# Performance work log

Measured on AMD Instinct MI355X. Metric: run time of the kernel, lower is better.

## Reference

```python
import jax, jax.numpy as jnp
import numpy as np

H = 51  # n_hidden
B = 8192  # batch
T = 2048  # seq_len
FUTURE = 64


def setup_inputs() -> dict:
    key = jax.random.key(0)
    ks = jax.random.split(key, 12)
    s = 1.0 / np.sqrt(H)
    u = lambda k, shape: jax.random.uniform(k, shape, jnp.float32, -s, s)
    return {
        "x": jax.random.normal(ks[0], (B, T), jnp.float32),
        "W_ih1": u(ks[1], (4 * H, 1)),
        "W_hh1": u(ks[2], (4 * H, H)),
        "b_ih1": u(ks[3], (4 * H,)),
        "b_hh1": u(ks[4], (4 * H,)),
        "W_ih2": u(ks[5], (4 * H, H)),
        "W_hh2": u(ks[6], (4 * H, H)),
        "b_ih2": u(ks[7], (4 * H,)),
        "b_hh2": u(ks[8], (4 * H,)),
        "W_out": u(ks[9], (1, H)),
        "b_out": u(ks[10], (1,)),
        "future": FUTURE,
    }


def _lstm_cell(x, h, c, Wih, Whh, bih, bhh):
    # PyTorch LSTMCell: gates ordered i, f, g, o
    g = x @ Wih.T + h @ Whh.T + (bih + bhh)  # [B, 4H]
    i, f, gg, o = jnp.split(g, 4, axis=-1)
    i = jax.nn.sigmoid(i)
    f = jax.nn.sigmoid(f)
    gg = jnp.tanh(gg)
    o = jax.nn.sigmoid(o)
    c2 = f * c + i * gg
    h2 = o * jnp.tanh(c2)
    return h2, c2


def reference(x, W_ih1, W_hh1, b_ih1, b_hh1, W_ih2, W_hh2, b_ih2, b_hh2,
              W_out, b_out, future):
    Bn = x.shape[0]
    h1 = jnp.zeros((Bn, H), x.dtype)
    c1 = jnp.zeros((Bn, H), x.dtype)

    def emit(h1, c1):
        # Quirk of the original code: layer-2 state is layer-1's CURRENT (h1, c1),
        # and layer-2's own state is never carried forward.
        h2, _ = _lstm_cell(h1, h1, c1, W_ih2, W_hh2, b_ih2, b_hh2)
        return h2 @ W_out.T + b_out  # [B, 1]

    def step(carry, xt):
        h1, c1 = carry
        h1, c1 = _lstm_cell(xt, h1, c1, W_ih1, W_hh1, b_ih1, b_hh1)
        out = emit(h1, c1)
        return (h1, c1), out

    xs = jnp.swapaxes(x, 0, 1)[:, :, None]  # [T, B, 1]
    (h1, c1), outs = jax.lax.scan(step, (h1, c1), xs)
    outs = outs[..., 0].T  # [B, T]

    def fstep(carry, _):
        h1, c1, out = carry
        h1, c1 = _lstm_cell(out, h1, c1, W_ih1, W_hh1, b_ih1, b_hh1)
        out = emit(h1, c1)
        return (h1, c1, out), out

    last = outs[:, -1:]
    _, fouts = jax.lax.scan(fstep, (h1, c1, last), None, length=future)
    fouts = fouts[..., 0].T if future > 0 else jnp.zeros((Bn, 0), x.dtype)
    return jnp.concatenate([outs, fouts], axis=1)  # [B, T + future]
```

## Files before the change

### kernel.cpp

```cpp
#include <hip/hip_runtime.h>

#define HH   51
#define H4   204
#define TSEQ 2048
#define FUT  64
#define TT   (TSEQ + FUT)
#define RPB  16
#define NTH  1024
#define HSTR 80

typedef _Float16 h8 __attribute__((ext_vector_type(8)));
typedef float    f4 __attribute__((ext_vector_type(4)));

#define LOG2E 1.44269504f

__device__ __forceinline__ float sigm_f(float z) {
    return __builtin_amdgcn_rcpf(1.0f + __builtin_amdgcn_exp2f(-LOG2E * z));
}
__device__ __forceinline__ float tanh_f(float z) {
    return __builtin_fmaf(2.0f,
        __builtin_amdgcn_rcpf(1.0f + __builtin_amdgcn_exp2f(-2.0f * LOG2E * z)), -1.0f);
}

__global__ __launch_bounds__(NTH, 8)
void lstm_kernel(const float* __restrict__ x,
                 const float* __restrict__ Wih1, const float* __restrict__ Whh1,
                 const float* __restrict__ bih1, const float* __restrict__ bhh1,
                 const float* __restrict__ Wih2, const float* __restrict__ Whh2,
                 const float* __restrict__ bih2, const float* __restrict__ bhh2,
                 const float* __restrict__ Wout, const float* __restrict__ bout,
                 float* __restrict__ out)
{
    __shared__ _Float16 hbuf[2][RPB][HSTR];
    __shared__ float part[2][13][17];
    __shared__ float wouts[64];

    const int tid  = threadIdx.x;
    const int lane = tid & 63;
    const int w    = tid >> 6;
    const int quad = lane >> 4;
    const int nl   = lane & 15;
    const int rb   = blockIdx.x * RPB;

    if (tid < 64) wouts[tid] = (tid < HH) ? Wout[tid] : 0.0f;
    for (int i = tid; i < 2 * RPB * HSTR; i += NTH) (&hbuf[0][0][0])[i] = (_Float16)0.0f;
    __syncthreads();
    if (tid < RPB) {
        hbuf[0][tid][0]  = (_Float16)x[(size_t)(rb + tid) * TSEQ];
        hbuf[0][tid][52] = (_Float16)1.0f;  hbuf[0][tid][53] = (_Float16)1.0f;
        hbuf[1][tid][52] = (_Float16)1.0f;  hbuf[1][tid][53] = (_Float16)1.0f;
    }
    const float bo = bout[0];

    h8 W1[2], W2[2];
    if (w < 13) {
        const int jp = 16 * w + nl;
        const int kk = jp >> 2, q = jp & 3;
        const bool valid = (jp < H4);
        const int jrow = q * HH + kk;
        float b1 = 0.0f, b2 = 0.0f;
        if (valid) { b1 = bih1[jrow] + bhh1[jrow]; b2 = bih2[jrow] + bhh2[jrow]; }
        const _Float16 b1h = (_Float16)b1, b2h = (_Float16)b2;
        const _Float16 b1l = (_Float16)(b1 - (float)b1h), b2l = (_Float16)(b2 - (float)b2h);
        #pragma unroll
        for (int s = 0; s < 2; ++s) {
            h8 w1v, w2v;
            #pragma unroll
            for (int j = 0; j < 8; ++j) {
                const int k = s * 32 + quad * 8 + j;
                _Float16 a1 = (_Float16)0.0f, a2 = (_Float16)0.0f;
                if (valid) {
                    if (k == 0) {
                        a1 = (_Float16)Wih1[jrow];
                    } else if (k <= HH) {
                        const int o = jrow * HH + (k - 1);
                        a1 = (_Float16)Whh1[o];
                        a2 = (_Float16)(Wih2[o] + Whh2[o]);
                    } else if (k == 52) { a1 = b1h; a2 = b2h; }
                    else if (k == 53)   { a1 = b1l; a2 = b2l; }
                }
                w1v[j] = a1;
                w2v[j] = a2;
            }
            W1[s] = w1v;
            W2[s] = w2v;
        }
    }

    float xnext = 0.0f;
    if (w == 14 && lane < RPB) xnext = x[(size_t)(rb + lane) * TSEQ + 1];

    const int kh = 4 * w + quad;
    float c1 = 0.0f;
    __syncthreads();

    for (int t = 0; t < TT; ++t) {
        const int cur = t & 1, nxt = cur ^ 1;

        if (w < 13) {
            const h8 Bh0 = *(const h8*)&hbuf[cur][nl][quad * 8];
            const h8 Bh1 = *(const h8*)&hbuf[cur][nl][32 + quad * 8];
            f4 g = {0.f, 0.f, 0.f, 0.f};
            g = __builtin_amdgcn_mfma_f32_16x16x32_f16(W1[0], Bh0, g, 0, 0, 0);
            g = __builtin_amdgcn_mfma_f32_16x16x32_f16(W1[1], Bh1, g, 0, 0, 0);
            const float ig = sigm_f(g[0]);
            const float fg = sigm_f(g[1]);
            const float gg = tanh_f(g[2]);
            const float og = sigm_f(g[3]);
            c1 = fg * c1 + ig * gg;
            const float h1v = og * tanh_f(c1);
            if (kh < HH) hbuf[nxt][nl][1 + kh] = (_Float16)h1v;
        } else if (w == 13) {
            if (t >= 1 && t <= TSEQ - 1 && lane < RPB) {
                float s = bo;
                #pragma unroll
                for (int j = 0; j < 13; ++j) s += part[cur ^ 1][j][lane];
                out[(size_t)(rb + lane) * TT + (t - 1)] = s;
            }
        } else if (w == 14) {
            if (lane < RPB) {
                if (t + 1 < TSEQ) hbuf[nxt][lane][0] = (_Float16)xnext;
                if (t + 2 < TSEQ) xnext = x[(size_t)(rb + lane) * TSEQ + (t + 2)];
            }
        }
        __syncthreads();

        if (w < 13) {
            const h8 Bh0 = *(const h8*)&hbuf[nxt][nl][quad * 8];
            const h8 Bh1 = *(const h8*)&hbuf[nxt][nl][32 + quad * 8];
            f4 g = {0.f, 0.f, 0.f, 0.f};
            g = __builtin_amdgcn_mfma_f32_16x16x32_f16(W2[0], Bh0, g, 0, 0, 0);
            g = __builtin_amdgcn_mfma_f32_16x16x32_f16(W2[1], Bh1, g, 0, 0, 0);
            const float ig = sigm_f(g[0]);
            const float fg = sigm_f(g[1]);
            const float gg = tanh_f(g[2]);
            const float og = sigm_f(g[3]);
            const float c2 = fg * c1 + ig * gg;
            float p = og * tanh_f(c2) * wouts[kh];
            p += __shfl_xor(p, 16, 64);
            p += __shfl_xor(p, 32, 64);
            if (quad == 0) part[cur][w][nl] = p;
        }
        __syncthreads();

        if (t >= TSEQ - 1) {
            if (w == 13 && lane < RPB) {
                float s = bo;
                #pragma unroll
                for (int j = 0; j < 13; ++j) s += part[cur][j][lane];
                out[(size_t)(rb + lane) * TT + t] = s;
                hbuf[nxt][lane][0] = (_Float16)s;
            }
            __syncthreads();
        }
    }
}

extern "C" void kernel_launch(void* const* d_in, const int* in_sizes, int n_in,
                              void* d_out, int out_size, void* d_ws, size_t ws_size,
                              hipStream_t stream) {
    (void)in_sizes; (void)n_in; (void)d_ws; (void)ws_size; (void)out_size;
    const float* x    = (const float*)d_in[0];
    const float* Wih1 = (const float*)d_in[1];
    const float* Whh1 = (const float*)d_in[2];
    const float* bih1 = (const float*)d_in[3];
    const float* bhh1 = (const float*)d_in[4];
    const float* Wih2 = (const float*)d_in[5];
    const float* Whh2 = (const float*)d_in[6];
    const float* bih2 = (const float*)d_in[7];
    const float* bhh2 = (const float*)d_in[8];
    const float* Wout = (const float*)d_in[9];
    const float* bout = (const float*)d_in[10];
    float* outp = (float*)d_out;

    dim3 grid(8192 / RPB);
    dim3 block(NTH);
    hipLaunchKernelGGL(lstm_kernel, grid, block, 0, stream,
                       x, Wih1, Whh1, bih1, bhh1, Wih2, Whh2, bih2, bhh2,
                       Wout, bout, outp);
}
```

Before: 2.961 ms.

## Merge layer-1 and layer-2 LSTM phases into one barrier per step

```diff
diff --git a/kernel.cpp b/kernel.cpp
--- a/kernel.cpp
+++ b/kernel.cpp
@@ -13,14 +13,57 @@
 typedef float    f4 __attribute__((ext_vector_type(4)));
 
 #define LOG2E 1.44269504f
-
-__device__ __forceinline__ float sigm_f(float z) {
-    return __builtin_amdgcn_rcpf(1.0f + __builtin_amdgcn_exp2f(-LOG2E * z));
+#define MFMA(a, b, c) __builtin_amdgcn_mfma_f32_16x16x32_f16(a, b, c, 0, 0, 0)
+
+__device__ __forceinline__ void act_cell(const f4 g, float cin, float* cout, float* hout) {
+    const float ei = __builtin_amdgcn_exp2f(-LOG2E * g[0]);
+    const float ef = __builtin_amdgcn_exp2f(-LOG2E * g[1]);
+    const float eg = __builtin_amdgcn_exp2f(-2.0f * LOG2E * g[2]);
+    const float eo = __builtin_amdgcn_exp2f(-LOG2E * g[3]);
+    const float A = 1.0f + ei, B = 1.0f + ef, G = 1.0f + eg, C = 1.0f + eo;
+    const float rAB = __builtin_amdgcn_rcpf(A * B);
+    const float ig = rAB * B;
+    const float fg = rAB * A;
+    const float rGC = __builtin_amdgcn_rcpf(G * C);
+    const float og = rGC * G;
+    const float tg = __builtin_fmaf(2.0f, rGC * C, -1.0f);
+    const float c2 = __builtin_fmaf(fg, cin, ig * tg);
+    const float ec = __builtin_amdgcn_exp2f(-2.0f * LOG2E * c2);
+    const float th = __builtin_fmaf(2.0f, __builtin_amdgcn_rcpf(1.0f + ec), -1.0f);
+    *cout = c2;
+    *hout = og * th;
 }
-__device__ __forceinline__ float tanh_f(float z) {
-    return __builtin_fmaf(2.0f,
-        __builtin_amdgcn_rcpf(1.0f + __builtin_amdgcn_exp2f(-2.0f * LOG2E * z)), -1.0f);
-}
+
+#define MERGED_BODY(P, EMIT_IDX, DO_EMIT, XI)                                      \
+    do {                                                                           \
+        if (is_comp) {                                                             \
+            const h8 b0 = *(const h8*)&hbuf[P][nl][quad * 8];                      \
+            const h8 b1 = *(const h8*)&hbuf[P][nl][32 + quad * 8];                 \
+            f4 G1 = {0.f, 0.f, 0.f, 0.f}, G2 = {0.f, 0.f, 0.f, 0.f};               \
+            G2 = MFMA(W2[0], b0, G2); G2 = MFMA(W2[1], b1, G2);                    \
+            G1 = MFMA(W1[0], b0, G1); G1 = MFMA(W1[1], b1, G1);                    \
+            float c2v, h2v;                                                        \
+            act_cell(G2, c1, &c2v, &h2v);         \
+            float p = h2v * wo;                                                    \
+            p += __shfl_xor(p, 16, 64);                                            \
+            p += __shfl_xor(p, 32, 64);                                            \
+            if (quad == 0) part[(P) ^ 1][cw][nl] = p;                              \
+            float hv;                                                              \
+            act_cell(G1, c1, &c1, &hv);                     \
+            if (kh < HH) hbuf[(P) ^ 1][nl][1 + kh] = (_Float16)hv;                 \
+        } else if (w == we) {                                                      \
+            if ((DO_EMIT) && lane < RPB) {                                         \
+                float s = bo;                                                      \
+                _Pragma("unroll")                                                  \
+                for (int j = 0; j < 13; ++j) s += part[P][j][lane];                \
+                out[(size_t)(rb + lane) * TT + (EMIT_IDX)] = s;                    \
+            }                                                                      \
+        } else if (w == wp && lane < RPB) {                                        \
+            if ((XI) + 1 < TSEQ) hbuf[(P) ^ 1][lane][0] = (_Float16)xnext;         \
+            if ((XI) + 2 < TSEQ) xnext = x[(size_t)(rb + lane) * TSEQ + (XI) + 2]; \
+        }                                                                          \
+        __syncthreads();                                                           \
+    } while (0)
 
 __global__ __launch_bounds__(NTH, 8)
 void lstm_kernel(const float* __restrict__ x,
@@ -42,6 +85,12 @@
     const int nl   = lane & 15;
     const int rb   = blockIdx.x * RPB;
 
+    const int  rot     = (blockIdx.x >> 8) & 1;
+    const int  cw      = w - (rot ? 3 : 0);
+    const bool is_comp = (cw >= 0) && (cw < 13);
+    const int  we      = rot ? 0 : 13;
+    const int  wp      = rot ? 1 : 14;
+
     if (tid < 64) wouts[tid] = (tid < HH) ? Wout[tid] : 0.0f;
     for (int i = tid; i < 2 * RPB * HSTR; i += NTH) (&hbuf[0][0][0])[i] = (_Float16)0.0f;
     __syncthreads();
@@ -53,8 +102,8 @@
     const float bo = bout[0];
 
     h8 W1[2], W2[2];
-    if (w < 13) {
-        const int jp = 16 * w + nl;
+    if (is_comp) {
+        const int jp = 16 * cw + nl;
         const int kk = jp >> 2, q = jp & 3;
         const bool valid = (jp < H4);
         const int jrow = q * HH + kk;
@@ -88,68 +137,71 @@
     }
 
     float xnext = 0.0f;
-    if (w == 14 && lane < RPB) xnext = x[(size_t)(rb + lane) * TSEQ + 1];
-
-    const int kh = 4 * w + quad;
+    if (w == wp && lane < RPB) xnext = x[(size_t)(rb + lane) * TSEQ + 1];
+
+    const int kh = 4 * cw + quad;
     float c1 = 0.0f;
     __syncthreads();
-
-    for (int t = 0; t < TT; ++t) {
-        const int cur = t & 1, nxt = cur ^ 1;
-
-        if (w < 13) {
-            const h8 Bh0 = *(const h8*)&hbuf[cur][nl][quad * 8];
-            const h8 Bh1 = *(const h8*)&hbuf[cur][nl][32 + quad * 8];
-            f4 g = {0.f, 0.f, 0.f, 0.f};
-            g = __builtin_amdgcn_mfma_f32_16x16x32_f16(W1[0], Bh0, g, 0, 0, 0);
-            g = __builtin_amdgcn_mfma_f32_16x16x32_f16(W1[1], Bh1, g, 0, 0, 0);
-            const float ig = sigm_f(g[0]);
-            const float fg = sigm_f(g[1]);
-            const float gg = tanh_f(g[2]);
-            const float og = sigm_f(g[3]);
-            c1 = fg * c1 + ig * gg;
-            const float h1v = og * tanh_f(c1);
-            if (kh < HH) hbuf[nxt][nl][1 + kh] = (_Float16)h1v;
-        } else if (w == 13) {
-            if (t >= 1 && t <= TSEQ - 1 && lane < RPB) {
-                float s = bo;
-                #pragma unroll
-                for (int j = 0; j < 13; ++j) s += part[cur ^ 1][j][lane];
-                out[(size_t)(rb + lane) * TT + (t - 1)] = s;
-            }
-        } else if (w == 14) {
-            if (lane < RPB) {
-                if (t + 1 < TSEQ) hbuf[nxt][lane][0] = (_Float16)xnext;
-                if (t + 2 < TSEQ) xnext = x[(size_t)(rb + lane) * TSEQ + (t + 2)];
-            }
-        }
-        __syncthreads();
-
-        if (w < 13) {
-            const h8 Bh0 = *(const h8*)&hbuf[nxt][nl][quad * 8];
-            const h8 Bh1 = *(const h8*)&hbuf[nxt][nl][32 + quad * 8];
-            f4 g = {0.f, 0.f, 0.f, 0.f};
-            g = __builtin_amdgcn_mfma_f32_16x16x32_f16(W2[0], Bh0, g, 0, 0, 0);
-            g = __builtin_amdgcn_mfma_f32_16x16x32_f16(W2[1], Bh1, g, 0, 0, 0);
-            const float ig = sigm_f(g[0]);
-            const float fg = sigm_f(g[1]);
-            const float gg = tanh_f(g[2]);
-            const float og = sigm_f(g[3]);
-            const float c2 = fg * c1 + ig * gg;
-            float p = og * tanh_f(c2) * wouts[kh];
+    const float wo = is_comp ? wouts[kh] : 0.0f;
+
+    if (is_comp) {
+        const h8 b0 = *(const h8*)&hbuf[0][nl][quad * 8];
+        const h8 b1 = *(const h8*)&hbuf[0][nl][32 + quad * 8];
+        f4 G1 = {0.f, 0.f, 0.f, 0.f};
+        G1 = MFMA(W1[0], b0, G1); G1 = MFMA(W1[1], b1, G1);
+        float hv;
+        act_cell(G1, c1, &c1, &hv);
+        if (kh < HH) hbuf[1][nl][1 + kh] = (_Float16)hv;
+    } else if (w == wp && lane < RPB) {
+        hbuf[1][lane][0] = (_Float16)xnext;
+        xnext = x[(size_t)(rb + lane) * TSEQ + 2];
+    }
+    __syncthreads();
+
+    MERGED_BODY(1, 0, false, 1);
+
+    for (int i = 2; i < TSEQ; i += 2) {
+        MERGED_BODY(0, i - 2, true, i);
+        MERGED_BODY(1, i - 1, true, i + 1);
+    }
+
+    for (int t = TSEQ - 1; t < TT; ++t) {
+        const int pb = (t + 1) & 1;
+        if (is_comp) {
+            const h8 b0 = *(const h8*)&hbuf[pb][nl][quad * 8];
+            const h8 b1 = *(const h8*)&hbuf[pb][nl][32 + quad * 8];
+            f4 G2 = {0.f, 0.f, 0.f, 0.f};
+            G2 = MFMA(W2[0], b0, G2); G2 = MFMA(W2[1], b1, G2);
+            float c2v, h2v;
+            act_cell(G2, c1, &c2v, &h2v);
+            float p = h2v * wo;
             p += __shfl_xor(p, 16, 64);
             p += __shfl_xor(p, 32, 64);
-            if (quad == 0) part[cur][w][nl] = p;
+            if (quad == 0) part[t & 1][cw][nl] = p;
+        } else if (w == we && t == TSEQ - 1 && lane < RPB) {
+            float s = bo;
+            #pragma unroll
+            for (int j = 0; j < 13; ++j) s += part[0][j][lane];
+            out[(size_t)(rb + lane) * TT + (TSEQ - 2)] = s;
         }
         __syncthreads();
-
-        if (t >= TSEQ - 1) {
-            if (w == 13 && lane < RPB) {
-                float s = bo;
-                #pragma unroll
-                for (int j = 0; j < 13; ++j) s += part[cur][j][lane];
-                out[(size_t)(rb + lane) * TT + t] = s;
-                hbuf[nxt][lane][0] = (_Float16)s;
+        if (w == we && lane < RPB) {
+            float s = bo;
+            #pragma unroll
+            for (int j = 0; j < 13; ++j) s += part[t & 1][j][lane];
+            out[(size_t)(rb + lane) * TT + t] = s;
+            if (t + 1 < TT) hbuf[pb][lane][0] = (_Float16)s;
+        }
+        __syncthreads();
+        if (t + 1 < TT) {
+            if (is_comp) {
+                const h8 b0 = *(const h8*)&hbuf[pb][nl][quad * 8];
+                const h8 b1 = *(const h8*)&hbuf[pb][nl][32 + quad * 8];
+                f4 G1 = {0.f, 0.f, 0.f, 0.f};
+                G1 = MFMA(W1[0], b0, G1); G1 = MFMA(W1[1], b1, G1);
+                float hv;
+                act_cell(G1, c1, &c1, &hv);
+                if (kh < HH) hbuf[pb ^ 1][nl][1 + kh] = (_Float16)hv;
             }
             __syncthreads();
         }
```

Result: faster. 2.768 ms (-6.5%).
